# Optimization experiments

Hardware: AMD Instinct MI355X
Metric: run time of the kernel (lower is better)

## Reference

```python
import jax, jax.numpy as jnp
import numpy as np

N_DIM = 8
NUM_GRID = 2 ** N_DIM  # 256 local lattice offsets


def _e8_basis_param():
    # nn.Parameter init: E8 generator matrix / 2
    b = np.array([
        [2, 0, 0, 0, 0, 0, 0, 0],
        [0, 2, 0, 0, 0, 0, 0, 0],
        [0, 0, 2, 0, 0, 0, 0, 0],
        [0, 0, 0, 2, 0, 0, 0, 0],
        [1, 1, 1, 0, 1, 0, 0, 0],
        [1, 0, 1, 1, 0, 1, 0, 0],
        [1, 0, 0, 1, 1, 0, 1, 0],
        [1, 0, 0, 0, 1, 1, 0, 1],
    ], dtype=np.float32) / 2.0
    return jnp.asarray(b)


def _make_grid():
    # torch.cartesian_prod of [0,1]*N: first dim varies slowest
    j = jnp.arange(NUM_GRID)[:, None]
    shifts = jnp.arange(N_DIM - 1, -1, -1)[None, :]
    return ((j >> shifts) & 1).astype(jnp.float32)  # [256, 8]


def _normalized_basis(basis_param):
    b = jnp.tril(basis_param)
    det = jnp.prod(jnp.diagonal(b))  # triangular -> product of diagonal
    return b / jnp.abs(det)


def _find_nearest(x, basis, grid):
    B, K = x.shape
    # sequential triangular basis reduction (static unroll over N=8 dims)
    us = []
    x_temp = x
    for i in range(N_DIM)[::-1]:
        ui = jnp.floor(x_temp[:, i] / basis[i, i])  # [B]
        us.append(ui)
        if i != 0:
            x_temp = x_temp[:, :i] - ui[:, None] * basis[i, :i][None, :]
    dot = jnp.stack(us[::-1], axis=1)  # [B, N]
    pts = dot[:, None, :] + grid[None, :, :]  # [B, 256, N]
    code_book = jnp.einsum('bjn,nk->bjk', pts, basis)  # [B, 256, K]
    # squared l2 distance: ||x||^2 + ||cb||^2 - 2 cb.x
    dist = (jnp.sum(x * x, axis=1)[:, None]
            + jnp.sum(code_book * code_book, axis=2)
            - 2.0 * jnp.einsum('bjk,bk->bj', code_book, x)) / K  # [B, 256]
    idx = jnp.argmin(dist, axis=-1)  # [B]
    # one-hot scatter + einsum combine == gather of nearest codeword
    x_hat = jnp.take_along_axis(code_book, idx[:, None, None], axis=1)[:, 0, :]
    return x_hat, dist


def setup_inputs() -> dict:
    key = jax.random.key(0)
    kx, = jax.random.split(key, 1)
    B = 131072
    x = jax.random.normal(kx, (B, N_DIM), dtype=jnp.float32)
    basis_param = _e8_basis_param()
    return {"x": x, "basis_param": basis_param, "training": 0}


def reference(x, basis_param, training):
    basis = _normalized_basis(basis_param)
    grid = _make_grid()
    x_hat, dist = _find_nearest(x, basis, grid)
    # eval path: return (x_hat, x_indexes, dist) with x_indexes == x_hat
    return (x_hat, x_hat, dist)
```

## Files before the change

kernel.cpp:

```cpp
#include <hip/hip_runtime.h>
#include <hip/hip_bf16.h>
#include <cstdint>

#define WAVES 4

typedef float fx4 __attribute__((ext_vector_type(4)));

__global__ __launch_bounds__(256) void lvq_main(
    const float* __restrict__ x,
    const float* __restrict__ bp,
    float* __restrict__ oxh0,
    float* __restrict__ oxh1,
    float* __restrict__ odist,
    int B)
{
    __shared__ __align__(16) float sbasis[8][8];
    __shared__ __align__(16) float sgrid[256][8];
    __shared__ __align__(16) float scg2[256];
    __shared__ __align__(16) fx4 sbufv[WAVES][64][8];

    const int tid  = threadIdx.x;
    const int lane = tid & 63;
    const int wid  = tid >> 6;

    if (tid < 64) {
        const int i = tid >> 3, k = tid & 7;
        float det = 1.f;
        #pragma unroll
        for (int d = 0; d < 8; ++d) det *= bp[d * 8 + d];
        const float ad = fabsf(det);
        sbasis[i][k] = (k <= i) ? (bp[i * 8 + k] / ad) : 0.f;
    }
    __syncthreads();

    {
        const int j = tid;
        float g[8];
        #pragma unroll
        for (int k = 0; k < 8; ++k) {
            float s = 0.f;
            #pragma unroll
            for (int n = 0; n < 8; ++n)
                if ((j >> (7 - n)) & 1) s += sbasis[n][k];
            g[k] = s;
            sgrid[j][k] = s;
        }
        float g2 = 0.f;
        #pragma unroll
        for (int k = 0; k < 8; ++k) g2 += g[k] * g[k];
        int t = j; t ^= t >> 1; t ^= t >> 2; t ^= t >> 4;
        scg2[t] = g2 * 0.125f;
    }
    __syncthreads();

    const int group = blockIdx.x * WAVES + wid;
    const int b0 = group * 64;
    if (b0 >= B) return;
    const int b = b0 + lane;

    const float4* xp = reinterpret_cast<const float4*>(x + (size_t)b * 8);
    const float4 xa = xp[0], xb_ = xp[1];
    float xv[8] = {xa.x, xa.y, xa.z, xa.w, xb_.x, xb_.y, xb_.z, xb_.w};

    float xt[8];
    #pragma unroll
    for (int k = 0; k < 8; ++k) xt[k] = xv[k];
    float r[8];
    #pragma unroll
    for (int i = 7; i >= 0; --i) {
        const float bii = sbasis[i][i];
        const float ui = floorf(xt[i] / bii);
        r[i] = xt[i] - ui * bii;
        #pragma unroll
        for (int k = 0; k < i; ++k) xt[k] -= ui * sbasis[i][k];
    }
    float C = 0.f;
    #pragma unroll
    for (int k = 0; k < 8; ++k) C += r[k] * r[k];
    C *= 0.125f;
    float w[8];
    #pragma unroll
    for (int k = 0; k < 8; ++k) w[k] = -0.25f * r[k];
    float bnw[8];
    #pragma unroll
    for (int n = 0; n < 8; ++n) {
        float s = 0.f;
        #pragma unroll
        for (int k = 0; k <= n; ++k) s += sbasis[n][k] * w[k];
        bnw[n] = s;
    }

    float acc = 0.f;
    float md = 3.4e38f;
    int jmin = 0;
    const int g = lane & 7, K = lane >> 3;
    int jb_prev = 0, fix2_prev = 0;

    for (int c = 0; c < 8; ++c) {
        if (c) {
            const int p2 = __builtin_ctz(c);
            const float delta = (p2 == 0) ? bnw[2] : ((p2 == 1) ? bnw[1] : bnw[0]);
            const int gb = ((c ^ (c >> 1)) >> p2) & 1;
            acc = gb ? (acc + delta) : (acc - delta);
        }
        const int jb   = (c ^ (c >> 1)) << 5;
        const int fix4 = (c & 1) << 4;
        const int fix2 = (c & 1) << 2;
        const float bn3s = (c & 1) ? -bnw[3] : bnw[3];

        fx4 fr[8];
        if (c > 0) {
            #pragma unroll
            for (int m = 0; m < 8; ++m)
                fr[m] = sbufv[wid][K + 8 * m][(g ^ fix2_prev) ^ K];
        }
        fx4* gdst_prev = reinterpret_cast<fx4*>(odist + (size_t)(b0 + K) * 256 + jb_prev) + g;

        #pragma unroll
        for (int m = 0; m < 8; ++m) {
            const float4 c4 = *reinterpret_cast<const float4*>(&scg2[c * 32 + m * 4]);
            const float cg[4] = {c4.x, c4.y, c4.z, c4.w};
            float va[4];
            #pragma unroll
            for (int s = 0; s < 4; ++s) {
                const int tp = 4 * m + s;
                if (tp == 16) {
                    acc += bn3s;
                } else if (tp > 0) {
                    const int p = __builtin_ctz(tp);
                    const int sgn = ((tp ^ (tp >> 1)) >> p) & 1;
                    const int n = 7 - p;
                    acc = sgn ? (acc + bnw[n]) : (acc - bnw[n]);
                }
                const float d = (C + cg[tp & 3]) + acc;
                const int slot2 = (s ^ (s >> 1)) ^ ((m & 1) << 1);
                va[slot2] = d;
                const int jlow = ((tp ^ (tp >> 1)) & 15) | (tp & 16);
                const int j = jb ^ fix4 ^ jlow;
                if (d < md) { md = d; jmin = j; }
            }
            const int Q = (m & 4) | ((m ^ (m >> 1)) & 3);
            fx4 v4;
            v4.x = va[0]; v4.y = va[1]; v4.z = va[2]; v4.w = va[3];
            sbufv[wid][lane][Q ^ (lane & 7)] = v4;

            if (c > 0) gdst_prev[m * 512] = fr[m];
        }
        jb_prev = jb; fix2_prev = fix2;
    }
    {
        fx4* gdst = reinterpret_cast<fx4*>(odist + (size_t)(b0 + K) * 256 + jb_prev) + g;
        #pragma unroll
        for (int m = 0; m < 8; ++m) {
            const fx4 vf = sbufv[wid][K + 8 * m][(g ^ fix2_prev) ^ K];
            gdst[m * 512] = vf;
        }
    }

    const float4 ga = *reinterpret_cast<const float4*>(&sgrid[jmin][0]);
    const float4 gb2 = *reinterpret_cast<const float4*>(&sgrid[jmin][4]);
    const float gm[8] = {ga.x, ga.y, ga.z, ga.w, gb2.x, gb2.y, gb2.z, gb2.w};
    float xh[8];
    #pragma unroll
    for (int k = 0; k < 8; ++k) xh[k] = (xv[k] - r[k]) + gm[k];
    const float4 h0 = make_float4(xh[0], xh[1], xh[2], xh[3]);
    const float4 h1 = make_float4(xh[4], xh[5], xh[6], xh[7]);
    reinterpret_cast<float4*>(oxh0 + (size_t)b * 8)[0] = h0;
    reinterpret_cast<float4*>(oxh0 + (size_t)b * 8)[1] = h1;
    reinterpret_cast<float4*>(oxh1 + (size_t)b * 8)[0] = h0;
    reinterpret_cast<float4*>(oxh1 + (size_t)b * 8)[1] = h1;
}

extern "C" void kernel_launch(void* const* d_in, const int* in_sizes, int n_in,
                              void* d_out, int out_size, void* d_ws, size_t ws_size,
                              hipStream_t stream) {
    const float* x  = (const float*)d_in[0];
    const float* bp = (const float*)d_in[1];
    const int B = in_sizes[0] / 8;
    float* out   = (float*)d_out;
    float* oxh0  = out;
    float* oxh1  = out + (size_t)B * 8;
    float* odist = out + (size_t)2 * B * 8;
    const int groups = (B + 63) / 64;
    const int blocks = (groups + WAVES - 1) / WAVES;
    lvq_main<<<blocks, 256, 0, stream>>>(x, bp, oxh0, oxh1, odist, B);
}
```

Before: 29.36 us.

## Split into row-params kernel and coalesced distance-writing kernel via workspace

Splits the fused kernel in two. The first kernel computes per-row reduction parameters (C and the eight bnw values), the argmin and x_hat, and writes 12 floats per row to a workspace. The second kernel has each wave write one full 256-entry distance row with coalesced float4 stores, rebuilding the distances from those parameters and the precomputed grid norms, with no LDS transposition. The aim is simpler, fully coalesced writes of the large dist output, at the cost of an extra launch and a round trip through the workspace. The old fused kernel remains as a fallback when the workspace is too small.

```diff
diff --git a/kernel.cpp b/kernel.cpp
--- a/kernel.cpp
+++ b/kernel.cpp
@@ -6,7 +6,221 @@
 
 typedef float fx4 __attribute__((ext_vector_type(4)));
 
-__global__ __launch_bounds__(256) void lvq_main(
+__global__ __launch_bounds__(256) void lvq_rows(
+    const float* __restrict__ x,
+    const float* __restrict__ bp,
+    float* __restrict__ oxh0,
+    float* __restrict__ oxh1,
+    float* __restrict__ pbuf,
+    int B)
+{
+    __shared__ __align__(16) float sbasis[8][8];
+    __shared__ __align__(16) float sgrid[256][8];
+    __shared__ __align__(16) float scg2[256];
+
+    const int tid  = threadIdx.x;
+    const int lane = tid & 63;
+    const int wid  = tid >> 6;
+
+    if (tid < 64) {
+        const int i = tid >> 3, k = tid & 7;
+        float det = 1.f;
+        #pragma unroll
+        for (int d = 0; d < 8; ++d) det *= bp[d * 8 + d];
+        const float ad = fabsf(det);
+        sbasis[i][k] = (k <= i) ? (bp[i * 8 + k] / ad) : 0.f;
+    }
+    __syncthreads();
+
+    {
+        const int j = tid;
+        float g[8];
+        #pragma unroll
+        for (int k = 0; k < 8; ++k) {
+            float s = 0.f;
+            #pragma unroll
+            for (int n = 0; n < 8; ++n)
+                if ((j >> (7 - n)) & 1) s += sbasis[n][k];
+            g[k] = s;
+            sgrid[j][k] = s;
+        }
+        float g2 = 0.f;
+        #pragma unroll
+        for (int k = 0; k < 8; ++k) g2 += g[k] * g[k];
+        int t = j; t ^= t >> 1; t ^= t >> 2; t ^= t >> 4;
+        scg2[t] = g2 * 0.125f;
+    }
+    __syncthreads();
+
+    const int group = blockIdx.x * WAVES + wid;
+    const int b0 = group * 64;
+    if (b0 >= B) return;
+    const int b = b0 + lane;
+
+    const float4* xp = reinterpret_cast<const float4*>(x + (size_t)b * 8);
+    const float4 xa = xp[0], xb_ = xp[1];
+    float xv[8] = {xa.x, xa.y, xa.z, xa.w, xb_.x, xb_.y, xb_.z, xb_.w};
+
+    float xt[8];
+    #pragma unroll
+    for (int k = 0; k < 8; ++k) xt[k] = xv[k];
+    float r[8];
+    #pragma unroll
+    for (int i = 7; i >= 0; --i) {
+        const float bii = sbasis[i][i];
+        const float ui = floorf(xt[i] / bii);
+        r[i] = xt[i] - ui * bii;
+        #pragma unroll
+        for (int k = 0; k < i; ++k) xt[k] -= ui * sbasis[i][k];
+    }
+    float C = 0.f;
+    #pragma unroll
+    for (int k = 0; k < 8; ++k) C += r[k] * r[k];
+    C *= 0.125f;
+    float w[8];
+    #pragma unroll
+    for (int k = 0; k < 8; ++k) w[k] = -0.25f * r[k];
+    float bnw[8];
+    #pragma unroll
+    for (int n = 0; n < 8; ++n) {
+        float s = 0.f;
+        #pragma unroll
+        for (int k = 0; k <= n; ++k) s += sbasis[n][k] * w[k];
+        bnw[n] = s;
+    }
+
+    {
+        fx4 q0; q0.x = C;      q0.y = bnw[0]; q0.z = bnw[1]; q0.w = bnw[2];
+        fx4 q1; q1.x = bnw[3]; q1.y = bnw[4]; q1.z = bnw[5]; q1.w = bnw[6];
+        fx4 q2; q2.x = bnw[7]; q2.y = 0.f;    q2.z = 0.f;    q2.w = 0.f;
+        fx4* pd = reinterpret_cast<fx4*>(pbuf + (size_t)b * 12);
+        pd[0] = q0; pd[1] = q1; pd[2] = q2;
+    }
+
+    float acc = 0.f;
+    float md = 3.4e38f;
+    int jmin = 0;
+    for (int c = 0; c < 8; ++c) {
+        if (c) {
+            const int p2 = __builtin_ctz(c);
+            const float delta = (p2 == 0) ? bnw[2] : ((p2 == 1) ? bnw[1] : bnw[0]);
+            const int gb = ((c ^ (c >> 1)) >> p2) & 1;
+            acc = gb ? (acc + delta) : (acc - delta);
+        }
+        const int jb   = (c ^ (c >> 1)) << 5;
+        const int fix4 = (c & 1) << 4;
+        const float bn3s = (c & 1) ? -bnw[3] : bnw[3];
+        #pragma unroll
+        for (int m = 0; m < 8; ++m) {
+            const float4 c4 = *reinterpret_cast<const float4*>(&scg2[c * 32 + m * 4]);
+            const float cg[4] = {c4.x, c4.y, c4.z, c4.w};
+            #pragma unroll
+            for (int s = 0; s < 4; ++s) {
+                const int tp = 4 * m + s;
+                if (tp == 16) {
+                    acc += bn3s;
+                } else if (tp > 0) {
+                    const int p = __builtin_ctz(tp);
+                    const int sgn = ((tp ^ (tp >> 1)) >> p) & 1;
+                    const int n = 7 - p;
+                    acc = sgn ? (acc + bnw[n]) : (acc - bnw[n]);
+                }
+                const float d = (C + cg[tp & 3]) + acc;
+                const int jlow = ((tp ^ (tp >> 1)) & 15) | (tp & 16);
+                const int j = jb ^ fix4 ^ jlow;
+                if (d < md) { md = d; jmin = j; }
+            }
+        }
+    }
+
+    const float4 ga = *reinterpret_cast<const float4*>(&sgrid[jmin][0]);
+    const float4 gb2 = *reinterpret_cast<const float4*>(&sgrid[jmin][4]);
+    const float gm[8] = {ga.x, ga.y, ga.z, ga.w, gb2.x, gb2.y, gb2.z, gb2.w};
+    float xh[8];
+    #pragma unroll
+    for (int k = 0; k < 8; ++k) xh[k] = (xv[k] - r[k]) + gm[k];
+    const float4 h0 = make_float4(xh[0], xh[1], xh[2], xh[3]);
+    const float4 h1 = make_float4(xh[4], xh[5], xh[6], xh[7]);
+    reinterpret_cast<float4*>(oxh0 + (size_t)b * 8)[0] = h0;
+    reinterpret_cast<float4*>(oxh0 + (size_t)b * 8)[1] = h1;
+    reinterpret_cast<float4*>(oxh1 + (size_t)b * 8)[0] = h0;
+    reinterpret_cast<float4*>(oxh1 + (size_t)b * 8)[1] = h1;
+}
+
+__global__ __launch_bounds__(512) void lvq_dist(
+    const float* __restrict__ bp,
+    const float* __restrict__ pbuf,
+    float* __restrict__ odist,
+    int B)
+{
+    __shared__ __align__(16) float sbasis[8][8];
+    __shared__ __align__(16) float scg2lin[256];
+
+    const int tid  = threadIdx.x;
+    const int lane = tid & 63;
+    const int wid  = tid >> 6;
+
+    if (tid < 64) {
+        const int i = tid >> 3, k = tid & 7;
+        float det = 1.f;
+        #pragma unroll
+        for (int d = 0; d < 8; ++d) det *= bp[d * 8 + d];
+        const float ad = fabsf(det);
+        sbasis[i][k] = (k <= i) ? (bp[i * 8 + k] / ad) : 0.f;
+    }
+    __syncthreads();
+    if (tid < 256) {
+        const int j = tid;
+        float g2 = 0.f;
+        #pragma unroll
+        for (int k = 0; k < 8; ++k) {
+            float s = 0.f;
+            #pragma unroll
+            for (int n = 0; n < 8; ++n)
+                if ((j >> (7 - n)) & 1) s += sbasis[n][k];
+            g2 += s * s;
+        }
+        scg2lin[j] = g2 * 0.125f;
+    }
+    __syncthreads();
+
+    float fb[6];
+    #pragma unroll
+    for (int n = 0; n < 6; ++n) fb[n] = (float)((lane >> (5 - n)) & 1);
+    const fx4 cgv = *reinterpret_cast<const fx4*>(&scg2lin[4 * lane]);
+
+    const int gw = blockIdx.x * 8 + wid;
+    const int waves_total = gridDim.x * 8;
+
+    for (int it = 0; it < 8; ++it) {
+        const int row = gw + it * waves_total;
+        if (row >= B) break;
+        const fx4* pd = reinterpret_cast<const fx4*>(pbuf + (size_t)row * 12);
+        const fx4 a  = pd[0];
+        const fx4 bq = pd[1];
+        const fx4 q2 = pd[2];
+        const float b7 = q2.x;
+        float base = a.x;
+        base = fmaf(fb[0], a.y, base);
+        base = fmaf(fb[1], a.z, base);
+        base = fmaf(fb[2], a.w, base);
+        base = fmaf(fb[3], bq.x, base);
+        base = fmaf(fb[4], bq.y, base);
+        base = fmaf(fb[5], bq.z, base);
+        const float t7  = base + b7;
+        const float t6  = base + bq.w;
+        const float t67 = t6 + b7;
+        fx4 v;
+        v.x = base + cgv.x;
+        v.y = t7  + cgv.y;
+        v.z = t6  + cgv.z;
+        v.w = t67 + cgv.w;
+        fx4* gdst = reinterpret_cast<fx4*>(odist + (size_t)row * 256);
+        gdst[lane] = v;
+    }
+}
+
+__global__ __launch_bounds__(256) void lvq_fused(
     const float* __restrict__ x,
     const float* __restrict__ bp,
     float* __restrict__ oxh0,
@@ -32,7 +246,6 @@
         sbasis[i][k] = (k <= i) ? (bp[i * 8 + k] / ad) : 0.f;
     }
     __syncthreads();
-
     {
         const int j = tid;
         float g[8];
@@ -143,7 +356,6 @@
             fx4 v4;
             v4.x = va[0]; v4.y = va[1]; v4.z = va[2]; v4.w = va[3];
             sbufv[wid][lane][Q ^ (lane & 7)] = v4;
-
             if (c > 0) gdst_prev[m * 512] = fr[m];
         }
         jb_prev = jb; fix2_prev = fix2;
@@ -182,6 +394,15 @@
     float* oxh1  = out + (size_t)B * 8;
     float* odist = out + (size_t)2 * B * 8;
     const int groups = (B + 63) / 64;
-    const int blocks = (groups + WAVES - 1) / WAVES;
-    lvq_main<<<blocks, 256, 0, stream>>>(x, bp, oxh0, oxh1, odist, B);
+    const int blocks1 = (groups + WAVES - 1) / WAVES;
+
+    const size_t pneed = (size_t)B * 12 * sizeof(float);
+    if (ws_size >= pneed) {
+        float* pbuf = (float*)d_ws;
+        lvq_rows<<<blocks1, 256, 0, stream>>>(x, bp, oxh0, oxh1, pbuf, B);
+        const int blocks2 = 2048;
+        lvq_dist<<<blocks2, 512, 0, stream>>>(bp, pbuf, odist, B);
+    } else {
+        lvq_fused<<<blocks1, 256, 0, stream>>>(x, bp, oxh0, oxh1, odist, B);
+    }
 }
```

Measured after the change: 48.96 us. +66.7%, slower.
